# Kernel tuning notes

Hardware: AMD Instinct MI355X
Metric: run time of the kernel (lower is better)

The kernel has to match this reference:

```python
import jax, jax.numpy as jnp
import numpy as np

N = 15000000
BSZ = 4096
D = 2048
GAMMA = 0.8
TAU_INIT = 0.5
TAU_MIN = 0.05
TAU_MAX = 1.0
RHO = 0.8
ETA_INIT = 0.001
BETA_U = 0.9
GRAD_CLIP = 3.0


def setup_inputs() -> dict:
    key = jax.random.key(0)
    k1, k2 = jax.random.split(key)
    features = jax.random.normal(k1, (2 * BSZ, D), dtype=jnp.float32)
    index = jax.random.randint(k2, (BSZ,), 0, N)
    s = jnp.zeros((N,), jnp.float32)
    tau_buf = jnp.ones((N,), jnp.float32) * TAU_INIT
    u_buf = jnp.zeros((N,), jnp.float32)
    return {"features": features, "s": s, "tau_buf": tau_buf,
            "u_buf": u_buf, "index": index, "epoch": 1}


def reference(features, s, tau_buf, u_buf, index, epoch):
    B = features.shape[0] // 2
    num_neg = 2 * B - 2
    # F.normalize(features, dim=1)
    nrm = jnp.linalg.norm(features, axis=1, keepdims=True)
    f = features / jnp.maximum(nrm, 1e-12)
    sim = f @ f.T  # [2B, 2B]
    pos_sim = jnp.concatenate([jnp.diagonal(sim, offset=B),
                               jnp.diagonal(sim, offset=-B)])[:, None]  # [2B,1]
    tau = jnp.tile(tau_buf[index], 2)  # [2B]
    # sim_d_temps is detached in the torch code
    sim_d = jax.lax.stop_gradient(sim / tau[:, None])
    mask_neg = jnp.tile(1.0 - jnp.eye(B, dtype=sim.dtype), (2, 2))  # [2B,2B]
    exp_sd = jnp.exp(sim_d) * mask_neg
    g = jnp.sum(exp_sd, axis=1) / num_neg  # [2B]
    if epoch == 0:
        s1, s2 = g[:B], g[B:]
    else:
        s_old = s[index]
        s1 = (1.0 - GAMMA) * s_old + GAMMA * g[:B]
        s2 = (1.0 - GAMMA) * s_old + GAMMA * g[B:]
    s_new = s.at[index].set((s1 + s2) / 2.0)
    # s1/s2 derive from detached quantities + non-grad buffer in torch
    s1g = jax.lax.stop_gradient(s1)
    s2g = jax.lax.stop_gradient(s2)
    w1 = exp_sd[:B] / s1g[:, None]
    w2 = exp_sd[B:] / s2g[:, None]
    loss_1 = jnp.sum(w1 * sim[:B], axis=1, keepdims=True) / num_neg - pos_sim[:B]
    loss_2 = jnp.sum(w2 * sim[B:], axis=1, keepdims=True) / num_neg - pos_sim[B:]
    loss = (loss_1 + loss_2).mean()
    # temperature (tau) gradient estimate and buffer updates
    gt1 = jnp.log(s1g) + RHO - jnp.sum(w1 * sim_d[:B], axis=1) / num_neg
    gt2 = jnp.log(s2g) + RHO - jnp.sum(w2 * sim_d[B:], axis=1) / num_neg
    grad_tau = jnp.clip((gt1 + gt2) / 2.0, -GRAD_CLIP, GRAD_CLIP)
    u_new = (1.0 - BETA_U) * u_buf[index] + BETA_U * grad_tau
    tau_new = jnp.clip(tau_buf[index] - ETA_INIT * u_new, TAU_MIN, TAU_MAX)
    u_buf_new = u_buf.at[index].set(u_new)
    tau_buf_new = tau_buf.at[index].set(tau_new)
    return loss, s_new, u_buf_new, tau_buf_new
```

## Files before the change

### kernel.cpp

```cpp
#include <hip/hip_runtime.h>
#include <hip/hip_bf16.h>
#include <stdint.h>

#define B_SZ   4096
#define TWO_B  8192
#define D_DIM  2048
#define N_TOT  15000000
#define RHO    0.8f
#define NT     32
#define NJOB   1056
#define GT     512
#define INV_SC (1.0f/256.0f)

typedef __attribute__((ext_vector_type(4))) float f32x4;

__device__ __forceinline__ float waveReduceSum(float v) {
#pragma unroll
    for (int off = 32; off >= 1; off >>= 1) v += __shfl_down(v, off, 64);
    return v;
}
__device__ __forceinline__ void gload_lds16(const void* g, void* l) {
    __builtin_amdgcn_global_load_lds(
        (const __attribute__((address_space(1))) void*)(uintptr_t)g,
        (__attribute__((address_space(3))) void*)(uintptr_t)l,
        16, 0, 0);
}
__device__ __forceinline__ unsigned pk4(float a, float b, float c, float d) {
    int r = 0;
    r = __builtin_amdgcn_cvt_pk_fp8_f32(a, b, r, false);
    r = __builtin_amdgcn_cvt_pk_fp8_f32(c, d, r, true);
    return (unsigned)r;
}

__global__ __launch_bounds__(256) void knorm2(const float* __restrict__ feat,
                                              unsigned char* __restrict__ f8,
                                              float* __restrict__ posdot) {
    int i = blockIdx.x;
    int tid = threadIdx.x;
    const float4* ra = reinterpret_cast<const float4*>(feat + (size_t)i * D_DIM);
    const float4* rb = reinterpret_cast<const float4*>(feat + (size_t)(i + B_SZ) * D_DIM);
    float4 a0 = ra[tid * 2], a1 = ra[tid * 2 + 1];
    float4 b0 = rb[tid * 2], b1 = rb[tid * 2 + 1];
    float sa = a0.x*a0.x + a0.y*a0.y + a0.z*a0.z + a0.w*a0.w
             + a1.x*a1.x + a1.y*a1.y + a1.z*a1.z + a1.w*a1.w;
    float sb = b0.x*b0.x + b0.y*b0.y + b0.z*b0.z + b0.w*b0.w
             + b1.x*b1.x + b1.y*b1.y + b1.z*b1.z + b1.w*b1.w;
    float dp = a0.x*b0.x + a0.y*b0.y + a0.z*b0.z + a0.w*b0.w
             + a1.x*b1.x + a1.y*b1.y + a1.z*b1.z + a1.w*b1.w;
    sa = waveReduceSum(sa);
    sb = waveReduceSum(sb);
    dp = waveReduceSum(dp);
    __shared__ float wsum[3][4];
    if ((tid & 63) == 0) {
        int wv = tid >> 6;
        wsum[0][wv] = sa; wsum[1][wv] = sb; wsum[2][wv] = dp;
    }
    __syncthreads();
    float ta = wsum[0][0] + wsum[0][1] + wsum[0][2] + wsum[0][3];
    float tb = wsum[1][0] + wsum[1][1] + wsum[1][2] + wsum[1][3];
    float td = wsum[2][0] + wsum[2][1] + wsum[2][2] + wsum[2][3];
    float ia = 1.0f / fmaxf(sqrtf(ta), 1e-12f);
    float ib = 1.0f / fmaxf(sqrtf(tb), 1e-12f);
    if (tid == 0) posdot[i] = td * ia * ib;
    float xa = ia * 16.0f, xb = ib * 16.0f;
    uint2 oa, ob;
    oa.x = pk4(a0.x * xa, a0.y * xa, a0.z * xa, a0.w * xa);
    oa.y = pk4(a1.x * xa, a1.y * xa, a1.z * xa, a1.w * xa);
    ob.x = pk4(b0.x * xb, b0.y * xb, b0.z * xb, b0.w * xb);
    ob.y = pk4(b1.x * xb, b1.y * xb, b1.z * xb, b1.w * xb);
    reinterpret_cast<uint2*>(f8 + (size_t)i * D_DIM)[tid] = oa;
    reinterpret_cast<uint2*>(f8 + (size_t)(i + B_SZ) * D_DIM)[tid] = ob;
}

__global__ __launch_bounds__(GT, 4) void kgram(
        const unsigned char* __restrict__ f8,
        const float* __restrict__ tau_buf, const int* __restrict__ index,
        float* __restrict__ E, float* __restrict__ F,
        const float4* __restrict__ sIn, const float4* __restrict__ uIn,
        const float4* __restrict__ tIn, float* __restrict__ out) {
    const int raw = (int)blockIdx.x;
    const int bid = (raw & 7) * (NJOB / 8) + (raw >> 3);
    int C = (int)((sqrtf((float)(4 * bid + 1)) - 1.0f) * 0.5f);
    while (C * C + C > bid) --C;
    while ((C + 1) * (C + 1) + (C + 1) <= bid) ++C;
    const int R = bid - C * C - C;
    const int r0 = R * 128, c0 = C * 256;

    const int tid = threadIdx.x;
    const int lane = tid & 63;
    const int w = tid >> 6;
    const int wr = w >> 2;
    const int wc = w & 3;
    const int l15 = lane & 15, lhi = lane >> 4;

    __shared__ alignas(16) unsigned char As[3][128 * 64];
    __shared__ alignas(16) unsigned char Bs[3][256 * 64];

    f32x4 acc[4][4] = {};

    const int rr = lane >> 2;
    const int sj = (lane & 3) ^ ((rr >> 1) & 3);
    const size_t gA  = (size_t)(r0 + w * 16 + rr) * D_DIM + sj * 16;
    const size_t gB0 = (size_t)(c0 + w * 32 + rr) * D_DIM + sj * 16;
    const size_t gB1 = gB0 + 16 * D_DIM;
    const int lA = w * 1024, lB0 = w * 2048, lB1 = w * 2048 + 1024;

#define STAGE(buf, t)                                              \
    do {                                                           \
        size_t k_ = (size_t)(t) * 64u;                             \
        gload_lds16(f8 + gA + k_,  &As[buf][lA]);                  \
        gload_lds16(f8 + gB0 + k_, &Bs[buf][lB0]);                 \
        gload_lds16(f8 + gB1 + k_, &Bs[buf][lB1]);                 \
    } while (0)

    STAGE(0, 0);
    STAGE(1, 1);
    asm volatile("s_waitcnt vmcnt(3)" ::: "memory");
    __builtin_amdgcn_sched_barrier(0);
    __builtin_amdgcn_s_barrier();

    const int kx = (l15 >> 1) & 3;
    const int pk0 = (((lhi >> 1) ^ kx) * 16) + (lhi & 1) * 8;
    const int pk1 = ((((lhi >> 1) + 2) ^ kx) * 16) + (lhi & 1) * 8;

    int bufc = 0;
    for (int t = 0; t < NT; ++t) {
        if (t + 2 < NT) {
            int bw = (bufc >= 1) ? bufc - 1 : 2;
            STAGE(bw, t + 2);
        }
        const unsigned char* __restrict__ A_l = &As[bufc][0];
        const unsigned char* __restrict__ B_l = &Bs[bufc][0];
        long af[4][2], bfr[4][2];
#pragma unroll
        for (int m = 0; m < 4; ++m) {
            int rowb = (wr * 64 + m * 16 + l15) * 64;
            af[m][0] = *reinterpret_cast<const long*>(&A_l[rowb + pk0]);
            af[m][1] = *reinterpret_cast<const long*>(&A_l[rowb + pk1]);
        }
#pragma unroll
        for (int n = 0; n < 4; ++n) {
            int rowb = (wc * 64 + n * 16 + l15) * 64;
            bfr[n][0] = *reinterpret_cast<const long*>(&B_l[rowb + pk0]);
            bfr[n][1] = *reinterpret_cast<const long*>(&B_l[rowb + pk1]);
        }
        __builtin_amdgcn_s_setprio(1);
#pragma unroll
        for (int m = 0; m < 4; ++m)
#pragma unroll
            for (int n = 0; n < 4; ++n) {
                acc[m][n] = __builtin_amdgcn_mfma_f32_16x16x32_fp8_fp8(af[m][0], bfr[n][0], acc[m][n], 0, 0, 0);
                acc[m][n] = __builtin_amdgcn_mfma_f32_16x16x32_fp8_fp8(af[m][1], bfr[n][1], acc[m][n], 0, 0, 0);
            }
        __builtin_amdgcn_s_setprio(0);
        if (t < NT - 2) {
            asm volatile("s_waitcnt vmcnt(3)" ::: "memory");
        } else if (t == NT - 2) {
            asm volatile("s_waitcnt vmcnt(0)" ::: "memory");
        }
        __builtin_amdgcn_sched_barrier(0);
        if (t < NT - 1) __builtin_amdgcn_s_barrier();
        bufc = (bufc == 2) ? 0 : bufc + 1;
    }
#undef STAGE

#pragma unroll
    for (int m = 0; m < 4; ++m) {
#pragma unroll
        for (int r = 0; r < 4; ++r) {
            int row_g = r0 + wr * 64 + m * 16 + lhi * 4 + r;
            float it = 1.0f / tau_buf[index[row_g & (B_SZ - 1)]];
            float e = 0.f, f = 0.f;
#pragma unroll
            for (int n = 0; n < 4; ++n) {
                int col_g = c0 + wc * 64 + n * 16 + l15;
                float v = acc[m][n][r] * INV_SC;
                if (col_g > row_g && (((row_g ^ col_g) & (B_SZ - 1)) != 0)) {
                    float ex = __expf(v * it);
                    e += ex;
                    f += ex * v;
                }
            }
#pragma unroll
            for (int off = 1; off < 16; off <<= 1) {
                e += __shfl_xor(e, off, 64);
                f += __shfl_xor(f, off, 64);
            }
            if (l15 == 0) {
                atomicAdd(&E[row_g], e);
                atomicAdd(&F[row_g], f);
            }
        }
    }
#pragma unroll
    for (int n = 0; n < 4; ++n) {
        int colT = c0 + wc * 64 + n * 16 + l15;
        float it = 1.0f / tau_buf[index[colT & (B_SZ - 1)]];
        float e = 0.f, f = 0.f;
#pragma unroll
        for (int m = 0; m < 4; ++m) {
#pragma unroll
            for (int r = 0; r < 4; ++r) {
                int row_g = r0 + wr * 64 + m * 16 + lhi * 4 + r;
                float v = acc[m][n][r] * INV_SC;
                if (colT > row_g && (((row_g ^ colT) & (B_SZ - 1)) != 0)) {
                    float ex = __expf(v * it);
                    e += ex;
                    f += ex * v;
                }
            }
        }
        e += __shfl_xor(e, 16, 64);
        f += __shfl_xor(f, 16, 64);
        e += __shfl_xor(e, 32, 64);
        f += __shfl_xor(f, 32, 64);
        if (lhi == 0) {
            atomicAdd(&E[colT], e);
            atomicAdd(&F[colT], f);
        }
    }

    {
        typedef float4 __attribute__((aligned(4))) float4u;
        size_t i = (size_t)raw * GT + tid;
        const size_t stride = (size_t)NJOB * GT;
        const size_t n4 = N_TOT / 4;
        for (; i < n4; i += stride) {
            *reinterpret_cast<float4u*>(out + 1 + 4 * i) = sIn[i];
            *reinterpret_cast<float4u*>(out + 1 + (size_t)N_TOT + 4 * i) = uIn[i];
            *reinterpret_cast<float4u*>(out + 1 + 2 * (size_t)N_TOT + 4 * i) = tIn[i];
        }
    }
}

__global__ __launch_bounds__(64) void kfin(const float* __restrict__ E,
                                           const float* __restrict__ F,
                                           const float* __restrict__ posdot,
                                           const float* __restrict__ s,
                                           const float* __restrict__ tau_buf,
                                           const float* __restrict__ u_buf,
                                           const int* __restrict__ index,
                                           const int* __restrict__ epoch_p,
                                           float* __restrict__ out) {
    int i = blockIdx.x;
    int lane = threadIdx.x;
    int idx = index[i];
    bool dup = false;
    for (int j = i + 1 + lane; j < B_SZ; j += 64)
        if (index[j] == idx) dup = true;
    unsigned long long ball = __ballot(dup);

    if (lane == 0) {
        float e1 = E[i], f1 = F[i];
        float e2 = E[i + B_SZ], f2 = F[i + B_SZ];
        const float num_neg = 2.0f * B_SZ - 2.0f;
        float g1 = e1 / num_neg, g2 = e2 / num_neg;
        float s_old = s[idx];
        float tau_i = tau_buf[idx];
        float u_old = u_buf[idx];
        int ep = *epoch_p;
        float s1, s2;
        if (ep == 0) { s1 = g1; s2 = g2; }
        else { s1 = 0.2f * s_old + 0.8f * g1; s2 = 0.2f * s_old + 0.8f * g2; }
        float pos = posdot[i];
        float l1 = f1 / (s1 * num_neg) - pos;
        float l2 = f2 / (s2 * num_neg) - pos;
        atomicAdd(out, (l1 + l2) * (1.0f / B_SZ));
        float gt1 = logf(s1) + RHO - f1 / (tau_i * s1 * num_neg);
        float gt2 = logf(s2) + RHO - f2 / (tau_i * s2 * num_neg);
        float gt = 0.5f * (gt1 + gt2);
        gt = fminf(fmaxf(gt, -3.0f), 3.0f);
        float u_new = 0.1f * u_old + 0.9f * gt;
        float tau_new = fminf(fmaxf(tau_i - 0.001f * u_new, 0.05f), 1.0f);
        if (ball == 0ULL) {
            out[1 + (size_t)idx] = 0.5f * (s1 + s2);
            out[1 + (size_t)N_TOT + idx] = u_new;
            out[1 + 2 * (size_t)N_TOT + idx] = tau_new;
        }
    }
}

extern "C" void kernel_launch(void* const* d_in, const int* in_sizes, int n_in,
                              void* d_out, int out_size, void* d_ws, size_t ws_size,
                              hipStream_t stream) {
    const float* features = (const float*)d_in[0];
    const float* s        = (const float*)d_in[1];
    const float* tau_buf  = (const float*)d_in[2];
    const float* u_buf    = (const float*)d_in[3];
    const int*   index    = (const int*)d_in[4];
    const int*   epoch    = (const int*)d_in[5];
    float* out = (float*)d_out;
    char* ws = (char*)d_ws;

    unsigned char* f8     = (unsigned char*)(ws);
    float*         E      = (float*)(ws + 16777216);
    float*         F      = (float*)(ws + 16809984);
    float*         posdot = (float*)(ws + 16842752);

    hipMemsetAsync(d_out, 0, sizeof(float), stream);
    hipMemsetAsync(E, 0, 2 * TWO_B * sizeof(float), stream);

    knorm2<<<B_SZ, 256, 0, stream>>>(features, f8, posdot);
    kgram<<<NJOB, GT, 0, stream>>>(f8, tau_buf, index, E, F,
                                   (const float4*)s, (const float4*)u_buf,
                                   (const float4*)tau_buf, out);
    kfin<<<B_SZ, 64, 0, stream>>>(E, F, posdot, s, tau_buf, u_buf, index, epoch, out);
}
```

Baseline: 303.4 us.

## Split tail gram tiles into fine-grained sliver kernel to balance load

Lowers the main gram kernel's job count from 1056 to 1024 and adds a separate sliver kernel with 256 blocks. Each sliver block computes a 16-row by 256-column strip of the last column tile band using FP8 MFMA with triple-buffered LDS staging, then atomically accumulates the exp sums into E and F. The aim is to remove the tail imbalance where a handful of large jobs run alone after the rest of the grid has finished. In exchange it adds a kernel launch and more atomics, and correctness depends on the job remapping in kgram matching the new NJOB.

```diff
diff --git a/kernel.cpp b/kernel.cpp
--- a/kernel.cpp
+++ b/kernel.cpp
@@ -8,7 +8,8 @@
 #define N_TOT  15000000
 #define RHO    0.8f
 #define NT     32
-#define NJOB   1056
+#define NJOB   1024
+#define NSLV   256
 #define GT     512
 #define INV_SC (1.0f/256.0f)
 
@@ -229,6 +230,140 @@
             *reinterpret_cast<float4u*>(out + 1 + 4 * i) = sIn[i];
             *reinterpret_cast<float4u*>(out + 1 + (size_t)N_TOT + 4 * i) = uIn[i];
             *reinterpret_cast<float4u*>(out + 1 + 2 * (size_t)N_TOT + 4 * i) = tIn[i];
+        }
+    }
+}
+
+__global__ __launch_bounds__(GT, 4) void ksliver(
+        const unsigned char* __restrict__ f8,
+        const float* __restrict__ tau_buf, const int* __restrict__ index,
+        float* __restrict__ E, float* __restrict__ F) {
+    const int sb = (int)blockIdx.x;
+    const int R = 32 + (sb >> 3);
+    const int sv = sb & 7;
+    const int r0 = R * 128 + sv * 16;
+    const int c0 = 31 * 256;
+
+    const int tid = threadIdx.x;
+    const int lane = tid & 63;
+    const int w = tid >> 6;
+    const int l15 = lane & 15, lhi = lane >> 4;
+
+    __shared__ alignas(16) unsigned char As[3][16 * 64];
+    __shared__ alignas(16) unsigned char Bs[3][256 * 64];
+
+    f32x4 acc[2] = {};
+
+    const int rr = lane >> 2;
+    const int sj = (lane & 3) ^ ((rr >> 1) & 3);
+    const size_t gA  = (size_t)(r0 + rr) * D_DIM + sj * 16;
+    const size_t gB0 = (size_t)(c0 + w * 32 + rr) * D_DIM + sj * 16;
+    const size_t gB1 = gB0 + 16 * D_DIM;
+    const int lB0 = w * 2048, lB1 = w * 2048 + 1024;
+
+#define STAGE(buf, t)                                              \
+    do {                                                           \
+        size_t k_ = (size_t)(t) * 64u;                             \
+        gload_lds16(f8 + gA + k_,  &As[buf][0]);                   \
+        gload_lds16(f8 + gB0 + k_, &Bs[buf][lB0]);                 \
+        gload_lds16(f8 + gB1 + k_, &Bs[buf][lB1]);                 \
+    } while (0)
+
+    STAGE(0, 0);
+    STAGE(1, 1);
+    asm volatile("s_waitcnt vmcnt(3)" ::: "memory");
+    __builtin_amdgcn_sched_barrier(0);
+    __builtin_amdgcn_s_barrier();
+
+    const int kx = (l15 >> 1) & 3;
+    const int pk0 = (((lhi >> 1) ^ kx) * 16) + (lhi & 1) * 8;
+    const int pk1 = ((((lhi >> 1) + 2) ^ kx) * 16) + (lhi & 1) * 8;
+
+    int bufc = 0;
+    for (int t = 0; t < NT; ++t) {
+        if (t + 2 < NT) {
+            int bw = (bufc >= 1) ? bufc - 1 : 2;
+            STAGE(bw, t + 2);
+        }
+        const unsigned char* __restrict__ A_l = &As[bufc][0];
+        const unsigned char* __restrict__ B_l = &Bs[bufc][0];
+        long af0, af1, bfr[2][2];
+        {
+            int rowb = l15 * 64;
+            af0 = *reinterpret_cast<const long*>(&A_l[rowb + pk0]);
+            af1 = *reinterpret_cast<const long*>(&A_l[rowb + pk1]);
+        }
+#pragma unroll
+        for (int n = 0; n < 2; ++n) {
+            int rowb = (w * 32 + n * 16 + l15) * 64;
+            bfr[n][0] = *reinterpret_cast<const long*>(&B_l[rowb + pk0]);
+            bfr[n][1] = *reinterpret_cast<const long*>(&B_l[rowb + pk1]);
+        }
+        __builtin_amdgcn_s_setprio(1);
+#pragma unroll
+        for (int n = 0; n < 2; ++n) {
+            acc[n] = __builtin_amdgcn_mfma_f32_16x16x32_fp8_fp8(af0, bfr[n][0], acc[n], 0, 0, 0);
+            acc[n] = __builtin_amdgcn_mfma_f32_16x16x32_fp8_fp8(af1, bfr[n][1], acc[n], 0, 0, 0);
+        }
+        __builtin_amdgcn_s_setprio(0);
+        if (t < NT - 2) {
+            asm volatile("s_waitcnt vmcnt(3)" ::: "memory");
+        } else if (t == NT - 2) {
+            asm volatile("s_waitcnt vmcnt(0)" ::: "memory");
+        }
+        __builtin_amdgcn_sched_barrier(0);
+        if (t < NT - 1) __builtin_amdgcn_s_barrier();
+        bufc = (bufc == 2) ? 0 : bufc + 1;
+    }
+#undef STAGE
+
+#pragma unroll
+    for (int r = 0; r < 4; ++r) {
+        int row_g = r0 + lhi * 4 + r;
+        float it = 1.0f / tau_buf[index[row_g & (B_SZ - 1)]];
+        float e = 0.f, f = 0.f;
+#pragma unroll
+        for (int n = 0; n < 2; ++n) {
+            int col_g = c0 + w * 32 + n * 16 + l15;
+            float v = acc[n][r] * INV_SC;
+            if (col_g > row_g && (((row_g ^ col_g) & (B_SZ - 1)) != 0)) {
+                float ex = __expf(v * it);
+                e += ex;
+                f += ex * v;
+            }
+        }
+#pragma unroll
+        for (int off = 1; off < 16; off <<= 1) {
+            e += __shfl_xor(e, off, 64);
+            f += __shfl_xor(f, off, 64);
+        }
+        if (l15 == 0) {
+            atomicAdd(&E[row_g], e);
+            atomicAdd(&F[row_g], f);
+        }
+    }
+#pragma unroll
+    for (int n = 0; n < 2; ++n) {
+        int colT = c0 + w * 32 + n * 16 + l15;
+        float it = 1.0f / tau_buf[index[colT & (B_SZ - 1)]];
+        float e = 0.f, f = 0.f;
+#pragma unroll
+        for (int r = 0; r < 4; ++r) {
+            int row_g = r0 + lhi * 4 + r;
+            float v = acc[n][r] * INV_SC;
+            if (colT > row_g && (((row_g ^ colT) & (B_SZ - 1)) != 0)) {
+                float ex = __expf(v * it);
+                e += ex;
+                f += ex * v;
+            }
+        }
+        e += __shfl_xor(e, 16, 64);
+        f += __shfl_xor(f, 16, 64);
+        e += __shfl_xor(e, 32, 64);
+        f += __shfl_xor(f, 32, 64);
+        if (lhi == 0) {
+            atomicAdd(&E[colT], e);
+            atomicAdd(&F[colT], f);
         }
     }
 }
@@ -304,5 +439,6 @@
     kgram<<<NJOB, GT, 0, stream>>>(f8, tau_buf, index, E, F,
                                    (const float4*)s, (const float4*)u_buf,
                                    (const float4*)tau_buf, out);
+    ksliver<<<NSLV, GT, 0, stream>>>(f8, tau_buf, index, E, F);
     kfin<<<B_SZ, 64, 0, stream>>>(E, F, posdot, s, tau_buf, u_buf, index, epoch, out);
 }
```

Measured after the change: 299.4 us. No clear change (-1.3%).
